# Optimization experiments

Measured on AMD Instinct MI355X. Metric: run time of the kernel, lower is better.

Reference implementation:

```python
import jax, jax.numpy as jnp
import numpy as np

NEG_SLOPE = 0.01  # torch F.leaky_relu default

def _leaky(x):
    return jnp.where(x >= 0, x, NEG_SLOPE * x)

def _gcn(x, W, b, src, dst, w, n):
    # GCNConv(add_self_loops=False, normalize=False):
    # h = x @ W; out[dst] += w * h[src]; out += b
    h = x @ W
    agg = jax.ops.segment_sum(w[:, None] * h[src], dst, num_segments=n)
    return agg + b

def setup_inputs() -> dict:
    key = jax.random.key(0)
    ks = jax.random.split(key, 10)
    N, E, IN, HID, OUT, B = 100000, 300000, 256, 256, 256, 128
    features = jax.random.normal(ks[0], (N, IN), dtype=jnp.float32)
    values = jax.random.uniform(ks[1], (E,), dtype=jnp.float32)
    s = 1.0 / np.sqrt(IN)
    W1 = jax.random.normal(ks[2], (IN, HID), dtype=jnp.float32) * s
    b1 = jnp.zeros((HID,), dtype=jnp.float32)
    W2 = jax.random.normal(ks[3], (HID + IN, OUT), dtype=jnp.float32) * (1.0 / np.sqrt(HID + IN))
    b2 = jnp.zeros((OUT,), dtype=jnp.float32)
    Wl = jax.random.normal(ks[4], (HID + OUT, IN), dtype=jnp.float32) * (1.0 / np.sqrt(HID + OUT))
    bl = jnp.zeros((IN,), dtype=jnp.float32)
    adjs = jax.random.randint(ks[5], (2, E), 0, N, dtype=jnp.int64)
    batch = jnp.sort(jax.random.randint(ks[6], (N,), 0, B, dtype=jnp.int64))
    root_idx = jax.random.randint(ks[7], (B,), 0, N, dtype=jnp.int64)
    return {"features": features, "values": values, "W1": W1, "b1": b1,
            "W2": W2, "b2": b2, "Wl": Wl, "bl": bl,
            "adjs": adjs, "batch": batch, "root_idx": root_idx}

def reference(features, values, W1, b1, W2, b2, Wl, bl, adjs, batch, root_idx):
    N = features.shape[0]
    src, dst = adjs[0], adjs[1]
    f1 = features  # [N, in]
    h = _gcn(f1, W1, b1, src, dst, values, N)  # conv1 -> [N, hid]
    f2 = h
    # root_extend: per-batch broadcast of root features == gather f1[root_idx[batch]]
    root1 = f1[root_idx[batch]]  # [N, in]
    x = _leaky(jnp.concatenate([h, root1], axis=1))
    # dropout is identity at inference
    x = _gcn(x, W2, b2, src, dst, values, N)  # conv2 -> [N, out]
    x = _leaky(x)
    root2 = f2[root_idx[batch]]  # [N, hid]
    x = jnp.concatenate([x, root2], axis=1)
    return _leaky(x @ Wl + bl)  # [N, in]
```

## Files before the change

### kernel.cpp

```cpp
#include <hip/hip_runtime.h>

typedef short short8 __attribute__((ext_vector_type(8)));
typedef float floatx4 __attribute__((ext_vector_type(4)));

#define LEAKY(v) ((v) >= 0.0f ? (v) : 0.01f * (v))

constexpr int D = 256;

__device__ __forceinline__ short f2bf(float x) {
  unsigned u = __float_as_uint(x);
  u += 0x7fffu + ((u >> 16) & 1u);
  return (short)(u >> 16);
}
__device__ __forceinline__ float bf2f(short s) {
  return __uint_as_float(((unsigned)(unsigned short)s) << 16);
}

__global__ void transpose_w(const float* __restrict__ W1,
                            const float* __restrict__ W2,
                            const float* __restrict__ Wl,
                            short* __restrict__ Wt) {
  __shared__ float t[32][33];
  const float* src = (blockIdx.z == 0) ? W1 : (blockIdx.z == 1) ? W2 : Wl;
  short* dst = Wt + (size_t)blockIdx.z * D * D;
  int tx = threadIdx.x, ty = threadIdx.y;
  t[ty][tx] = src[(size_t)(blockIdx.y * 32 + ty) * D + blockIdx.x * 32 + tx];
  __syncthreads();
  dst[(size_t)(blockIdx.x * 32 + ty) * D + blockIdx.y * 32 + tx] =
      f2bf(t[tx][ty]);
}

template <bool A_F32, bool ADD_ROW, bool FINAL>
__global__ __launch_bounds__(256) void gemm_mfma(
    const void* __restrict__ Avoid, const short* __restrict__ Wt,
    const float* __restrict__ R, const int* __restrict__ batch,
    const float* __restrict__ bias, void* __restrict__ Cvoid, int M) {
  __shared__ __align__(16) short As[64 * 72];
  __shared__ __align__(16) short Bs[256 * 72];
  const int tid = threadIdx.x;
  const int l = tid & 63, w = tid >> 6, lm = l & 15, q = l >> 4;
  const int rowBase = blockIdx.x * 64;

  floatx4 acc[4][4];
#pragma unroll
  for (int i = 0; i < 4; i++)
#pragma unroll
    for (int j = 0; j < 4; j++) acc[i][j] = (floatx4){0.f, 0.f, 0.f, 0.f};

  const int arow = tid >> 2;
  const int akseg = (tid & 3) * 16;

  for (int k0 = 0; k0 < D; k0 += 64) {
    {
      int grow = rowBase + arow;
      if (A_F32) {
        short8 s0 = {0, 0, 0, 0, 0, 0, 0, 0}, s1 = {0, 0, 0, 0, 0, 0, 0, 0};
        if (grow < M) {
          const float* ap = (const float*)Avoid + (size_t)grow * D + k0 + akseg;
          float4 v0 = ((const float4*)ap)[0];
          float4 v1 = ((const float4*)ap)[1];
          float4 v2 = ((const float4*)ap)[2];
          float4 v3 = ((const float4*)ap)[3];
          s0[0] = f2bf(v0.x); s0[1] = f2bf(v0.y); s0[2] = f2bf(v0.z); s0[3] = f2bf(v0.w);
          s0[4] = f2bf(v1.x); s0[5] = f2bf(v1.y); s0[6] = f2bf(v1.z); s0[7] = f2bf(v1.w);
          s1[0] = f2bf(v2.x); s1[1] = f2bf(v2.y); s1[2] = f2bf(v2.z); s1[3] = f2bf(v2.w);
          s1[4] = f2bf(v3.x); s1[5] = f2bf(v3.y); s1[6] = f2bf(v3.z); s1[7] = f2bf(v3.w);
        }
        *(short8*)(As + arow * 72 + akseg) = s0;
        *(short8*)(As + arow * 72 + akseg + 8) = s1;
      } else {
        uint4 u0 = {0, 0, 0, 0}, u1 = {0, 0, 0, 0};
        if (grow < M) {
          const uint4* ap =
              (const uint4*)((const short*)Avoid + (size_t)grow * D + k0 + akseg);
          u0 = ap[0];
          u1 = ap[1];
        }
        *(uint4*)(As + arow * 72 + akseg) = u0;
        *(uint4*)(As + arow * 72 + akseg + 8) = u1;
      }
    }
    {
      const uint4* wp = (const uint4*)(Wt + (size_t)tid * D + k0);
#pragma unroll
      for (int x = 0; x < 8; x++) *(uint4*)(Bs + tid * 72 + x * 8) = wp[x];
    }
    __syncthreads();
#pragma unroll
    for (int kk = 0; kk < 64; kk += 32) {
      short8 a[4], b[4];
#pragma unroll
      for (int i = 0; i < 4; i++)
        a[i] = *(const short8*)(As + (i * 16 + lm) * 72 + kk + q * 8);
#pragma unroll
      for (int j = 0; j < 4; j++)
        b[j] = *(const short8*)(Bs + (w * 64 + j * 16 + lm) * 72 + kk + q * 8);
#pragma unroll
      for (int i = 0; i < 4; i++)
#pragma unroll
        for (int j = 0; j < 4; j++)
          acc[i][j] = __builtin_amdgcn_mfma_f32_16x16x32_bf16(a[i], b[j],
                                                              acc[i][j], 0, 0, 0);
    }
    __syncthreads();
  }

#pragma unroll
  for (int i = 0; i < 4; i++) {
#pragma unroll
    for (int r = 0; r < 4; r++) {
      int row = rowBase + i * 16 + q * 4 + r;
      if (row < M) {
        int rb = 0;
        if (ADD_ROW) rb = batch[row];
        if (!FINAL) {
          short* C = (short*)Cvoid;
#pragma unroll
          for (int j = 0; j < 4; j++) {
            int col = w * 64 + j * 16 + lm;
            float c = acc[i][j][r];
            if (ADD_ROW) c += R[(size_t)rb * D + col];
            C[(size_t)row * D + col] = f2bf(c);
          }
        } else {
          float* C = (float*)Cvoid;
#pragma unroll
          for (int j = 0; j < 4; j++) {
            int col = w * 64 + j * 16 + lm;
            float c = acc[i][j][r];
            if (ADD_ROW) c += R[(size_t)rb * D + col];
            c += bias[col];
            c = LEAKY(c);
            C[(size_t)row * D + col] = c;
          }
        }
      }
    }
  }
}

__global__ void count_dst(const int* __restrict__ dst, int* __restrict__ offs,
                          int E) {
  int e = blockIdx.x * 256 + threadIdx.x;
  if (e < E) atomicAdd(&offs[dst[e]], 1);
}

__global__ void scan_blocks(int* __restrict__ offs, int* __restrict__ bsums,
                            int n) {
  __shared__ int tmp[256];
  int i = blockIdx.x * 256 + threadIdx.x;
  int v = (i < n) ? offs[i] : 0;
  tmp[threadIdx.x] = v;
  __syncthreads();
  for (int off = 1; off < 256; off <<= 1) {
    int t = (threadIdx.x >= off) ? tmp[threadIdx.x - off] : 0;
    __syncthreads();
    tmp[threadIdx.x] += t;
    __syncthreads();
  }
  if (i < n) offs[i] = tmp[threadIdx.x] - v;
  if (threadIdx.x == 255) bsums[blockIdx.x] = tmp[255];
}

__global__ void scan_sums(int* __restrict__ bs, int nb) {
  __shared__ int tmp[1024];
  int v = (threadIdx.x < nb) ? bs[threadIdx.x] : 0;
  tmp[threadIdx.x] = v;
  __syncthreads();
  for (int off = 1; off < 1024; off <<= 1) {
    int t = (threadIdx.x >= off) ? tmp[threadIdx.x - off] : 0;
    __syncthreads();
    tmp[threadIdx.x] += t;
    __syncthreads();
  }
  if (threadIdx.x < nb) bs[threadIdx.x] = tmp[threadIdx.x] - v;
}

__global__ void add_offsets(int* __restrict__ offs, const int* __restrict__ bs,
                            int n, int* __restrict__ cursor) {
  int i = blockIdx.x * 256 + threadIdx.x;
  if (i < n) {
    int o = offs[i] + bs[blockIdx.x];
    offs[i] = o;
    cursor[i] = o;
  }
}

__global__ void fill_buckets(const int* __restrict__ src,
                             const int* __restrict__ dst,
                             const float* __restrict__ vals,
                             int* __restrict__ cursor, int* __restrict__ esrc,
                             float* __restrict__ ew, int E) {
  int e = blockIdx.x * 256 + threadIdx.x;
  if (e < E) {
    int p = atomicAdd(&cursor[dst[e]], 1);
    esrc[p] = src[e];
    ew[p] = vals[e];
  }
}

__global__ __launch_bounds__(256) void aggregate_bf(
    const short* __restrict__ H, const int* __restrict__ offs,
    const int* __restrict__ esrc, const float* __restrict__ ew,
    const float* __restrict__ bias, short* __restrict__ out, int N, int E) {
  int node = blockIdx.x * 4 + (threadIdx.x >> 6);
  if (node >= N) return;
  int lane = threadIdx.x & 63;
  int beg = offs[node];
  int end = (node == N - 1) ? E : offs[node + 1];
  float a0 = 0.f, a1 = 0.f, a2 = 0.f, a3 = 0.f;
  for (int i = beg; i < end; i++) {
    int s = esrc[i];
    float wv = ew[i];
    uint2 pk = ((const uint2*)(H + (size_t)s * D))[lane];
    a0 += wv * bf2f((short)(pk.x & 0xffff));
    a1 += wv * bf2f((short)(pk.x >> 16));
    a2 += wv * bf2f((short)(pk.y & 0xffff));
    a3 += wv * bf2f((short)(pk.y >> 16));
  }
  float4 b = ((const float4*)bias)[lane];
  a0 = LEAKY(a0 + b.x);
  a1 = LEAKY(a1 + b.y);
  a2 = LEAKY(a2 + b.z);
  a3 = LEAKY(a3 + b.w);
  uint2 o;
  o.x = (unsigned)(unsigned short)f2bf(a0) |
        ((unsigned)(unsigned short)f2bf(a1) << 16);
  o.y = (unsigned)(unsigned short)f2bf(a2) |
        ((unsigned)(unsigned short)f2bf(a3) << 16);
  ((uint2*)(out + (size_t)node * D))[lane] = o;
}

__global__ void root_gemm1(const float* __restrict__ X,
                           const int* __restrict__ root_idx,
                           const float* __restrict__ W2,
                           float* __restrict__ R1) {
  __shared__ float a[D];
  int b = blockIdx.x, j = threadIdx.x;
  int r = root_idx[b];
  a[j] = LEAKY(X[(size_t)r * D + j]);
  __syncthreads();
  float acc = 0.f;
#pragma unroll 8
  for (int k = 0; k < D; k++) acc += a[k] * W2[(size_t)(D + k) * D + j];
  R1[b * D + j] = acc;
}

__global__ void root_gemm2(const short* __restrict__ H,
                           const int* __restrict__ root_idx,
                           const int* __restrict__ offs,
                           const int* __restrict__ esrc,
                           const float* __restrict__ ew,
                           const float* __restrict__ b1,
                           const float* __restrict__ Wl, float* __restrict__ R2,
                           int N, int E) {
  __shared__ float a[D];
  int b = blockIdx.x, j = threadIdx.x;
  int r = root_idx[b];
  int beg = offs[r], end = (r == N - 1) ? E : offs[r + 1];
  float acc = b1[j];
  for (int e = beg; e < end; e++)
    acc += ew[e] * bf2f(H[(size_t)esrc[e] * D + j]);
  a[j] = acc;
  __syncthreads();
  float s = 0.f;
#pragma unroll 8
  for (int k = 0; k < D; k++) s += a[k] * Wl[(size_t)(D + k) * D + j];
  R2[b * D + j] = s;
}

extern "C" void kernel_launch(void* const* d_in, const int* in_sizes, int n_in,
                              void* d_out, int out_size, void* d_ws,
                              size_t ws_size, hipStream_t stream) {
  const float* features = (const float*)d_in[0];
  const float* values   = (const float*)d_in[1];
  const float* W1 = (const float*)d_in[2];
  const float* b1 = (const float*)d_in[3];
  const float* W2 = (const float*)d_in[4];
  const float* b2 = (const float*)d_in[5];
  const float* Wl = (const float*)d_in[6];
  const float* bl = (const float*)d_in[7];
  const int* adjs = (const int*)d_in[8];
  const int* batch = (const int*)d_in[9];
  const int* root_idx = (const int*)d_in[10];

  const int N = in_sizes[0] / D;
  const int E = in_sizes[1];
  const int B = in_sizes[10];
  const int* srcI = adjs;
  const int* dstI = adjs + E;

  short* bf0 = (short*)d_ws;
  short* bf1 = bf0 + (size_t)N * D;
  short* Wt = bf1 + (size_t)N * D;
  float* R1 = (float*)(Wt + (size_t)3 * D * D);
  float* R2 = R1 + (size_t)B * D;
  float* ew = R2 + (size_t)B * D;
  int* offs = (int*)(ew + E);
  int* cursor = offs + N;
  int* esrc = cursor + N;
  int* bsums = esrc + E;

  const int nb = (N + 255) / 256;

  hipMemsetAsync(offs, 0, (size_t)N * sizeof(int), stream);
  count_dst<<<(E + 255) / 256, 256, 0, stream>>>(dstI, offs, E);
  scan_blocks<<<nb, 256, 0, stream>>>(offs, bsums, N);
  scan_sums<<<1, 1024, 0, stream>>>(bsums, nb);
  add_offsets<<<nb, 256, 0, stream>>>(offs, bsums, N, cursor);
  fill_buckets<<<(E + 255) / 256, 256, 0, stream>>>(srcI, dstI, values, cursor,
                                                    esrc, ew, E);

  transpose_w<<<dim3(8, 8, 3), dim3(32, 32), 0, stream>>>(W1, W2, Wl, Wt);

  const int ggrid = (N + 63) / 64;
  const int aggGrid = (N + 3) / 4;

  gemm_mfma<true, false, false><<<ggrid, 256, 0, stream>>>(
      features, Wt, nullptr, nullptr, nullptr, bf0, N);

  aggregate_bf<<<aggGrid, 256, 0, stream>>>(bf0, offs, esrc, ew, b1, bf1, N, E);

  root_gemm1<<<B, 256, 0, stream>>>(features, root_idx, W2, R1);
  root_gemm2<<<B, 256, 0, stream>>>(bf0, root_idx, offs, esrc, ew, b1, Wl, R2,
                                    N, E);

  gemm_mfma<false, true, false><<<ggrid, 256, 0, stream>>>(
      bf1, Wt + (size_t)D * D, R1, batch, nullptr, bf0, N);

  aggregate_bf<<<aggGrid, 256, 0, stream>>>(bf0, offs, esrc, ew, b2, bf1, N, E);

  gemm_mfma<false, true, true><<<ggrid, 256, 0, stream>>>(
      bf1, Wt + (size_t)2 * D * D, R2, batch, bl, (float*)d_out, N);
}
```

Baseline: 505.2 us.

## Replace LDS-tiled GEMM with persistent kernel holding weights in registers

The GEMM becomes persistent: 256 blocks of 512 threads loop over 64-row tiles. Each wave keeps its 32-column slice of the transposed bf16 weight matrix in registers for the whole kernel, so weights are loaded once per block instead of once per tile. A fragments are read directly from global memory into MFMA operands with no shared memory or barriers. This removes the per-tile weight reload and LDS round-trip, but it raises register pressure and makes A reads uncoalesced across the 8 waves, which each re-read the same rows.

New measurement: 665.3 us. 1.32x slower.

```diff
diff --git a/kernel.cpp b/kernel.cpp
--- a/kernel.cpp
+++ b/kernel.cpp
@@ -31,107 +31,81 @@
 }
 
 template <bool A_F32, bool ADD_ROW, bool FINAL>
-__global__ __launch_bounds__(256) void gemm_mfma(
+__global__ __launch_bounds__(512, 2) void gemm_persist(
     const void* __restrict__ Avoid, const short* __restrict__ Wt,
     const float* __restrict__ R, const int* __restrict__ batch,
-    const float* __restrict__ bias, void* __restrict__ Cvoid, int M) {
-  __shared__ __align__(16) short As[64 * 72];
-  __shared__ __align__(16) short Bs[256 * 72];
+    const float* __restrict__ bias, void* __restrict__ Cvoid, int M,
+    int nTiles) {
   const int tid = threadIdx.x;
   const int l = tid & 63, w = tid >> 6, lm = l & 15, q = l >> 4;
-  const int rowBase = blockIdx.x * 64;
-
-  floatx4 acc[4][4];
-#pragma unroll
-  for (int i = 0; i < 4; i++)
-#pragma unroll
-    for (int j = 0; j < 4; j++) acc[i][j] = (floatx4){0.f, 0.f, 0.f, 0.f};
-
-  const int arow = tid >> 2;
-  const int akseg = (tid & 3) * 16;
-
-  for (int k0 = 0; k0 < D; k0 += 64) {
-    {
-      int grow = rowBase + arow;
-      if (A_F32) {
-        short8 s0 = {0, 0, 0, 0, 0, 0, 0, 0}, s1 = {0, 0, 0, 0, 0, 0, 0, 0};
-        if (grow < M) {
-          const float* ap = (const float*)Avoid + (size_t)grow * D + k0 + akseg;
+  const int ncol0 = w * 32;
+
+  short8 bf[2][8];
+#pragma unroll
+  for (int j = 0; j < 2; j++)
+#pragma unroll
+    for (int kk = 0; kk < 8; kk++)
+      bf[j][kk] = *(const short8*)(Wt + (size_t)(ncol0 + j * 16 + lm) * D +
+                                   kk * 32 + q * 8);
+
+  const float* Af = (const float*)Avoid;
+  const short* Ab = (const short*)Avoid;
+
+  for (int t = blockIdx.x; t < nTiles; t += gridDim.x) {
+    const int rowBase = t * 64;
+    floatx4 acc[4][2];
+#pragma unroll
+    for (int i = 0; i < 4; i++)
+#pragma unroll
+      for (int j = 0; j < 2; j++) acc[i][j] = (floatx4){0.f, 0.f, 0.f, 0.f};
+
+#pragma unroll
+    for (int kk = 0; kk < 8; kk++) {
+      short8 a[4];
+#pragma unroll
+      for (int i = 0; i < 4; i++) {
+        int ar = rowBase + i * 16 + lm;
+        ar = ar < M ? ar : M - 1;
+        if (A_F32) {
+          const float* ap = Af + (size_t)ar * D + kk * 32 + q * 8;
           float4 v0 = ((const float4*)ap)[0];
           float4 v1 = ((const float4*)ap)[1];
-          float4 v2 = ((const float4*)ap)[2];
-          float4 v3 = ((const float4*)ap)[3];
-          s0[0] = f2bf(v0.x); s0[1] = f2bf(v0.y); s0[2] = f2bf(v0.z); s0[3] = f2bf(v0.w);
-          s0[4] = f2bf(v1.x); s0[5] = f2bf(v1.y); s0[6] = f2bf(v1.z); s0[7] = f2bf(v1.w);
-          s1[0] = f2bf(v2.x); s1[1] = f2bf(v2.y); s1[2] = f2bf(v2.z); s1[3] = f2bf(v2.w);
-          s1[4] = f2bf(v3.x); s1[5] = f2bf(v3.y); s1[6] = f2bf(v3.z); s1[7] = f2bf(v3.w);
+          short8 s;
+          s[0] = f2bf(v0.x); s[1] = f2bf(v0.y); s[2] = f2bf(v0.z); s[3] = f2bf(v0.w);
+          s[4] = f2bf(v1.x); s[5] = f2bf(v1.y); s[6] = f2bf(v1.z); s[7] = f2bf(v1.w);
+          a[i] = s;
+        } else {
+          a[i] = *(const short8*)(Ab + (size_t)ar * D + kk * 32 + q * 8);
         }
-        *(short8*)(As + arow * 72 + akseg) = s0;
-        *(short8*)(As + arow * 72 + akseg + 8) = s1;
-      } else {
-        uint4 u0 = {0, 0, 0, 0}, u1 = {0, 0, 0, 0};
-        if (grow < M) {
-          const uint4* ap =
-              (const uint4*)((const short*)Avoid + (size_t)grow * D + k0 + akseg);
-          u0 = ap[0];
-          u1 = ap[1];
-        }
-        *(uint4*)(As + arow * 72 + akseg) = u0;
-        *(uint4*)(As + arow * 72 + akseg + 8) = u1;
       }
+#pragma unroll
+      for (int i = 0; i < 4; i++)
+#pragma unroll
+        for (int j = 0; j < 2; j++)
+          acc[i][j] = __builtin_amdgcn_mfma_f32_16x16x32_bf16(
+              a[i], bf[j][kk], acc[i][j], 0, 0, 0);
     }
-    {
-      const uint4* wp = (const uint4*)(Wt + (size_t)tid * D + k0);
-#pragma unroll
-      for (int x = 0; x < 8; x++) *(uint4*)(Bs + tid * 72 + x * 8) = wp[x];
-    }
-    __syncthreads();
-#pragma unroll
-    for (int kk = 0; kk < 64; kk += 32) {
-      short8 a[4], b[4];
-#pragma unroll
-      for (int i = 0; i < 4; i++)
-        a[i] = *(const short8*)(As + (i * 16 + lm) * 72 + kk + q * 8);
-#pragma unroll
-      for (int j = 0; j < 4; j++)
-        b[j] = *(const short8*)(Bs + (w * 64 + j * 16 + lm) * 72 + kk + q * 8);
-#pragma unroll
-      for (int i = 0; i < 4; i++)
-#pragma unroll
-        for (int j = 0; j < 4; j++)
-          acc[i][j] = __builtin_amdgcn_mfma_f32_16x16x32_bf16(a[i], b[j],
-                                                              acc[i][j], 0, 0, 0);
-    }
-    __syncthreads();
-  }
-
-#pragma unroll
-  for (int i = 0; i < 4; i++) {
-#pragma unroll
-    for (int r = 0; r < 4; r++) {
-      int row = rowBase + i * 16 + q * 4 + r;
-      if (row < M) {
-        int rb = 0;
-        if (ADD_ROW) rb = batch[row];
-        if (!FINAL) {
-          short* C = (short*)Cvoid;
-#pragma unroll
-          for (int j = 0; j < 4; j++) {
-            int col = w * 64 + j * 16 + lm;
+
+#pragma unroll
+    for (int i = 0; i < 4; i++) {
+#pragma unroll
+      for (int r = 0; r < 4; r++) {
+        const int row = rowBase + i * 16 + q * 4 + r;
+        if (row < M) {
+          int rb = 0;
+          if (ADD_ROW) rb = batch[row];
+#pragma unroll
+          for (int j = 0; j < 2; j++) {
+            const int col = ncol0 + j * 16 + lm;
             float c = acc[i][j][r];
             if (ADD_ROW) c += R[(size_t)rb * D + col];
-            C[(size_t)row * D + col] = f2bf(c);
-          }
-        } else {
-          float* C = (float*)Cvoid;
-#pragma unroll
-          for (int j = 0; j < 4; j++) {
-            int col = w * 64 + j * 16 + lm;
-            float c = acc[i][j][r];
-            if (ADD_ROW) c += R[(size_t)rb * D + col];
-            c += bias[col];
-            c = LEAKY(c);
-            C[(size_t)row * D + col] = c;
+            if (!FINAL) {
+              ((short*)Cvoid)[(size_t)row * D + col] = f2bf(c);
+            } else {
+              c += bias[col];
+              c = LEAKY(c);
+              ((float*)Cvoid)[(size_t)row * D + col] = c;
+            }
           }
         }
       }
@@ -313,11 +287,12 @@
 
   transpose_w<<<dim3(8, 8, 3), dim3(32, 32), 0, stream>>>(W1, W2, Wl, Wt);
 
-  const int ggrid = (N + 63) / 64;
+  const int nTiles = (N + 63) / 64;
   const int aggGrid = (N + 3) / 4;
-
-  gemm_mfma<true, false, false><<<ggrid, 256, 0, stream>>>(
-      features, Wt, nullptr, nullptr, nullptr, bf0, N);
+  const int ggrid = 256;
+
+  gemm_persist<true, false, false><<<ggrid, 512, 0, stream>>>(
+      features, Wt, nullptr, nullptr, nullptr, bf0, N, nTiles);
 
   aggregate_bf<<<aggGrid, 256, 0, stream>>>(bf0, offs, esrc, ew, b1, bf1, N, E);
 
@@ -325,11 +300,11 @@
   root_gemm2<<<B, 256, 0, stream>>>(bf0, root_idx, offs, esrc, ew, b1, Wl, R2,
                                     N, E);
 
-  gemm_mfma<false, true, false><<<ggrid, 256, 0, stream>>>(
-      bf1, Wt + (size_t)D * D, R1, batch, nullptr, bf0, N);
+  gemm_persist<false, true, false><<<ggrid, 512, 0, stream>>>(
+      bf1, Wt + (size_t)D * D, R1, batch, nullptr, bf0, N, nTiles);
 
   aggregate_bf<<<aggGrid, 256, 0, stream>>>(bf0, offs, esrc, ew, b2, bf1, N, E);
 
-  gemm_mfma<false, true, true><<<ggrid, 256, 0, stream>>>(
-      bf1, Wt + (size_t)2 * D * D, R2, batch, bl, (float*)d_out, N);
-}
+  gemm_persist<false, true, true><<<ggrid, 512, 0, stream>>>(
+      bf1, Wt + (size_t)2 * D * D, R2, batch, bl, (float*)d_out, N, nTiles);
+}
```
